# Optimization experiments

Hardware: AMD Instinct MI355X
Metric: run time of the kernel (lower is better)

Reference implementation:

```python
import jax, jax.numpy as jnp
import numpy as np

N_VOX = 200000
C_IN = 64
C_OUT = 128
GRID = (480, 360, 32)  # (D, H, W) cylindrical voxel grid
LRELU_SLOPE = 0.01
BN_EPS = 1e-5

OFFSETS_31 = [(dz, 0, dx) for dz in (-1, 0, 1) for dx in (-1, 0, 1)]  # kernel (3,1,3)
OFFSETS_13 = [(0, dy, dx) for dy in (-1, 0, 1) for dx in (-1, 0, 1)]  # kernel (1,3,3)


def _build_neighbors(coords, offsets, grid):
    """coords: [N,3] int. Returns [K,N] int32 neighbor indices, N = sentinel (inactive)."""
    D, H, W = grid
    n = coords.shape[0]
    lookup = np.full(D * H * W, -1, dtype=np.int64)
    lin = (coords[:, 0] * H + coords[:, 1]) * W + coords[:, 2]
    lookup[lin] = np.arange(n)
    nbrs = []
    for off in offsets:
        c = coords + np.asarray(off)
        valid = (c[:, 0] >= 0) & (c[:, 0] < D) & (c[:, 1] >= 0) & (c[:, 1] < H) & (c[:, 2] >= 0) & (c[:, 2] < W)
        l = np.clip((c[:, 0] * H + c[:, 1]) * W + c[:, 2], 0, D * H * W - 1)
        idx = np.where(valid, lookup[l], -1)
        nbrs.append(np.where(idx < 0, n, idx))
    return np.stack(nbrs).astype(np.int32)


def setup_inputs() -> dict:
    key = jax.random.key(0)
    ks = jax.random.split(key, 8)
    rng = np.random.default_rng(0)
    D, H, W = GRID
    lin = rng.choice(D * H * W, size=N_VOX, replace=False)
    coords = np.stack([lin // (H * W), (lin // W) % H, lin % W], axis=1)
    nbr31 = jnp.asarray(_build_neighbors(coords, OFFSETS_31, GRID))
    nbr13 = jnp.asarray(_build_neighbors(coords, OFFSETS_13, GRID))

    def kaiming(k, kk, cin, cout):
        return jax.random.normal(k, (kk, cin, cout), jnp.float32) * np.float32(1.0 / np.sqrt(kk * cin))

    return {
        "features": jax.random.normal(ks[0], (N_VOX, C_IN), jnp.float32),
        "nbr31": nbr31,
        "nbr13": nbr13,
        "W_conv1": kaiming(ks[1], 9, C_IN, C_OUT),
        "W_conv1_2": kaiming(ks[2], 9, C_OUT, C_OUT),
        "W_conv2": kaiming(ks[3], 9, C_IN, C_OUT),
        "W_conv3": kaiming(ks[4], 9, C_OUT, C_OUT),
        "g0": jnp.ones((C_OUT,), jnp.float32), "b0": jnp.zeros((C_OUT,), jnp.float32),
        "g0_2": jnp.ones((C_OUT,), jnp.float32), "b0_2": jnp.zeros((C_OUT,), jnp.float32),
        "g1": jnp.ones((C_OUT,), jnp.float32), "b1": jnp.zeros((C_OUT,), jnp.float32),
        "g2": jnp.ones((C_OUT,), jnp.float32), "b2": jnp.zeros((C_OUT,), jnp.float32),
    }


def _submconv(f, nbr, W):
    """Submanifold sparse conv: f [N,Cin], nbr [K,N] (N=sentinel), W [K,Cin,Cout]."""
    f_pad = jnp.concatenate([f, jnp.zeros((1, f.shape[1]), f.dtype)], axis=0)
    out = jnp.zeros((f.shape[0], W.shape[2]), f.dtype)
    for k in range(W.shape[0]):  # fixed K=9 kernel taps
        out = out + f_pad[nbr[k]] @ W[k]
    return out


def _lrelu(x):
    return jnp.where(x >= 0, x, LRELU_SLOPE * x)


def _bn(x, g, b):
    # BatchNorm1d, training mode: batch stats over active voxels (biased var)
    m = jnp.mean(x, axis=0)
    v = jnp.var(x, axis=0)
    return (x - m) * jax.lax.rsqrt(v + BN_EPS) * g + b


def reference(features, nbr31, nbr13, W_conv1, W_conv1_2, W_conv2, W_conv3,
              g0, b0, g0_2, b0_2, g1, b1, g2, b2):
    # shortcut branch: conv3x1 -> lrelu -> bn -> conv1x3 -> lrelu -> bn
    s = _submconv(features, nbr31, W_conv1)
    s = _bn(_lrelu(s), g0, b0)
    s = _submconv(s, nbr13, W_conv1_2)
    s = _bn(_lrelu(s), g0_2, b0_2)
    # main branch: conv1x3 -> lrelu -> bn -> conv3x1 -> lrelu -> bn
    r = _submconv(features, nbr13, W_conv2)
    r = _bn(_lrelu(r), g1, b1)
    r = _submconv(r, nbr31, W_conv3)
    r = _bn(_lrelu(r), g2, b2)
    return r + s
```

## Files before the change

kernel.cpp:

```cpp
#include <hip/hip_runtime.h>
#include <hip/hip_bf16.h>

typedef unsigned short u16;
typedef unsigned int u32;
typedef __attribute__((ext_vector_type(8))) short s16x8;
typedef __attribute__((ext_vector_type(4))) short s16x4;
typedef __attribute__((ext_vector_type(4))) float f32x4;

__device__ inline u16 f2bf(float x) {
    u32 u = __float_as_uint(x);
    u32 r = (u + 0x7fffu + ((u >> 16) & 1u)) >> 16;
    return (u16)r;
}
__device__ inline float bf2f(u16 u) {
    return __uint_as_float(((u32)u) << 16);
}

__global__ void k_feat2bf(const float* __restrict__ f, u16* __restrict__ o,
                          int total, int nvalid) {
    int i = (blockIdx.x * 256 + threadIdx.x) * 8;
    if (i >= total) return;
    s16x8 v;
#pragma unroll
    for (int j = 0; j < 8; ++j) {
        float x = (i + j < nvalid) ? f[i + j] : 0.f;
        v[j] = (short)f2bf(x);
    }
    *(s16x8*)(o + i) = v;
}

__global__ void k_swz(const float* __restrict__ W, u16* __restrict__ o, int cin) {
    int i = blockIdx.x * 256 + threadIdx.x;
    int total = 9 * cin * 128;
    if (i >= total) return;
    int j = i & 7;
    int l = (i >> 3) & 63;
    int fr = i >> 9;
    int ct = fr & 7;
    int rest = fr >> 3;
    int kcn = cin >> 5;
    int kc = rest % kcn;
    int t = rest / kcn;
    int kk = kc * 32 + (l >> 4) * 8 + j;
    int c = ct * 16 + (l & 15);
    o[i] = f2bf(W[(t * cin + kk) * 128 + c]);
}

template <int CIN>
__global__ __launch_bounds__(1024, 4) void k_conv(
    const u16* __restrict__ srcA, const u16* __restrict__ srcB,
    const int* __restrict__ nbrA, const int* __restrict__ nbrB,
    const u16* __restrict__ wA, const u16* __restrict__ wB,
    u16* __restrict__ zoutA, u16* __restrict__ zoutB,
    float* __restrict__ statsA, float* __restrict__ statsB,
    int N) {
    constexpr int KC = CIN / 32;
    constexpr int FR = 9 * KC * 2;
    __shared__ u16 wl[FR * 512];
    __shared__ float sstat[64];

    const int nvr = (N + 511) >> 9;
    const int npairs = 2 * nvr;
    const int i = blockIdx.x;
    const int c8 = i & 7;
    const int m = i >> 3;
    const int h = m & 3;
    const int q = m >> 2;
    const int p = 8 * q + c8;
    if (p >= npairs) return;
    const int vr = p % nvr;
    const int cz = p / nvr;
    const int half = h;

    const u16* __restrict__ src = cz ? srcB : srcA;
    const int* __restrict__ nbr = cz ? nbrB : nbrA;
    const u16* __restrict__ w = cz ? wB : wA;
    u16* __restrict__ zout = cz ? zoutB : zoutA;
    float* __restrict__ stats = cz ? statsB : statsA;

    const int tid = threadIdx.x;

    for (int ii = tid; ii < FR * 64; ii += 1024) {
        int pp = ii & 63;
        int f = ii >> 6;
        int ctp = f & 1;
        int tk = f >> 1;
        s16x8 v = *(const s16x8*)(w + ((size_t)(tk * 8 + half * 2 + ctp)) * 512 + pp * 8);
        *(s16x8*)&wl[(size_t)f * 512 + pp * 8] = v;
    }
    if (tid < 64) sstat[tid] = 0.f;
    __syncthreads();

    const int lane = tid & 63;
    const int wv = tid >> 6;
    const int base = vr * 512 + wv * 32;
    const int am = lane & 15;
    const int grp = lane >> 4;
    const int vi0 = base + am;
    const int vi1 = base + 16 + am;

    int r0[9], r1[9];
#pragma unroll
    for (int t = 0; t < 9; ++t) {
        r0[t] = (vi0 < N) ? nbr[t * N + vi0] : N;
        r1[t] = (vi1 < N) ? nbr[t * N + vi1] : N;
    }

    f32x4 acc0[2], acc1[2];
#pragma unroll
    for (int c = 0; c < 2; ++c) {
        acc0[c] = (f32x4){0.f, 0.f, 0.f, 0.f};
        acc1[c] = (f32x4){0.f, 0.f, 0.f, 0.f};
    }

#pragma unroll
    for (int t = 0; t < 9; ++t) {
        if (__any((r0[t] != N) || (r1[t] != N))) {
            const u16* sp0 = src + (size_t)r0[t] * CIN + grp * 8;
            const u16* sp1 = src + (size_t)r1[t] * CIN + grp * 8;
            s16x8 a0[KC], a1[KC];
#pragma unroll
            for (int kc = 0; kc < KC; ++kc) {
                a0[kc] = *(const s16x8*)(sp0 + kc * 32);
                a1[kc] = *(const s16x8*)(sp1 + kc * 32);
            }
            const u16* lb = wl + (size_t)t * (KC * 2) * 512 + lane * 8;
#pragma unroll
            for (int kc = 0; kc < KC; ++kc) {
#pragma unroll
                for (int c = 0; c < 2; ++c) {
                    s16x8 b = *(const s16x8*)(lb + (kc * 2 + c) * 512);
                    acc0[c] = __builtin_amdgcn_mfma_f32_16x16x32_bf16(a0[kc], b, acc0[c], 0, 0, 0);
                    acc1[c] = __builtin_amdgcn_mfma_f32_16x16x32_bf16(a1[kc], b, acc1[c], 0, 0, 0);
                }
            }
        }
    }

#pragma unroll
    for (int c = 0; c < 2; ++c) {
        float s = 0.f, qq = 0.f;
        const int col = half * 32 + c * 16 + am;
#pragma unroll
        for (int j = 0; j < 4; ++j) {
            {
                float x = acc0[c][j];
                float z = (x > 0.f) ? x : 0.01f * x;
                int row = base + grp * 4 + j;
                if (row < N) zout[(size_t)row * 128 + col] = f2bf(z);
                s += z;
                qq += z * z;
            }
            {
                float x = acc1[c][j];
                float z = (x > 0.f) ? x : 0.01f * x;
                int row = base + 16 + grp * 4 + j;
                if (row < N) zout[(size_t)row * 128 + col] = f2bf(z);
                s += z;
                qq += z * z;
            }
        }
        s += __shfl_xor(s, 16);
        qq += __shfl_xor(qq, 16);
        s += __shfl_xor(s, 32);
        qq += __shfl_xor(qq, 32);
        if (lane < 16) {
            atomicAdd(&sstat[c * 16 + am], s);
            atomicAdd(&sstat[32 + c * 16 + am], qq);
        }
    }
    __syncthreads();
    if (tid < 32) {
        int cg = half * 32 + tid;
        atomicAdd(stats + cg, sstat[tid]);
        atomicAdd(stats + 128 + cg, sstat[32 + tid]);
    }
}

__global__ void k_fin(const float* __restrict__ stats,
                      const float* __restrict__ g0, const float* __restrict__ b0,
                      const float* __restrict__ g1, const float* __restrict__ b1,
                      float* __restrict__ ss, int N) {
    int tid = threadIdx.x;
    int set = tid >> 7, c = tid & 127;
    const float* st = stats + set * 256;
    float invN = 1.f / (float)N;
    float m = st[c] * invN;
    float var = st[128 + c] * invN - m * m;
    const float* g = set ? g1 : g0;
    const float* b = set ? b1 : b0;
    float sc = g[c] * rsqrtf(var + 1e-5f);
    float sh = b[c] - m * sc;
    float* o = ss + set * 256;
    o[c] = sc;
    o[128 + c] = sh;
}

__global__ void k_aff(const u16* __restrict__ z, const float* __restrict__ ss,
                      u16* __restrict__ y, int N) {
    int v = blockIdx.x * 256 + threadIdx.x;
    int total = (N + 1) * 16;
    if (v >= total) return;
    int row = v >> 4;
    int cb = (v & 15) * 8;
    s16x8 o;
    if (row < N) {
        s16x8 zi = *(const s16x8*)(z + (size_t)row * 128 + cb);
#pragma unroll
        for (int j = 0; j < 8; ++j) {
            float x = bf2f((u16)zi[j]);
            float r = x * ss[cb + j] + ss[128 + cb + j];
            o[j] = (short)f2bf(r);
        }
    } else {
        o = (s16x8){0, 0, 0, 0, 0, 0, 0, 0};
    }
    *(s16x8*)(y + (size_t)row * 128 + cb) = o;
}

__global__ void k_final(const u16* __restrict__ z3, const u16* __restrict__ z4,
                        const float* __restrict__ ssA, const float* __restrict__ ssB,
                        float* __restrict__ out, int N) {
    int v = blockIdx.x * 256 + threadIdx.x;
    int total = N * 32;
    if (v >= total) return;
    int row = v >> 5;
    int cb = (v & 31) * 4;
    s16x4 a = *(const s16x4*)(z3 + (size_t)row * 128 + cb);
    s16x4 b = *(const s16x4*)(z4 + (size_t)row * 128 + cb);
    f32x4 o;
#pragma unroll
    for (int j = 0; j < 4; ++j) {
        int c = cb + j;
        o[j] = bf2f((u16)a[j]) * ssA[c] + ssA[128 + c] +
               bf2f((u16)b[j]) * ssB[c] + ssB[128 + c];
    }
    *(f32x4*)(out + (size_t)row * 128 + cb) = o;
}

extern "C" void kernel_launch(void* const* d_in, const int* in_sizes, int n_in,
                              void* d_out, int out_size, void* d_ws, size_t ws_size,
                              hipStream_t stream) {
    const float* feat = (const float*)d_in[0];
    const int* nbr31 = (const int*)d_in[1];
    const int* nbr13 = (const int*)d_in[2];
    const float* W1 = (const float*)d_in[3];
    const float* W12 = (const float*)d_in[4];
    const float* W2 = (const float*)d_in[5];
    const float* W3 = (const float*)d_in[6];
    const float* g0 = (const float*)d_in[7];
    const float* b0 = (const float*)d_in[8];
    const float* g02 = (const float*)d_in[9];
    const float* b02 = (const float*)d_in[10];
    const float* g1 = (const float*)d_in[11];
    const float* b1 = (const float*)d_in[12];
    const float* g2 = (const float*)d_in[13];
    const float* b2 = (const float*)d_in[14];
    float* out = (float*)d_out;
    const int N = in_sizes[0] / 64;

    char* p = (char*)d_ws;
    auto alloc = [&](size_t bytes) {
        char* r = p;
        p += (bytes + 255) & ~(size_t)255;
        return r;
    };
    float* stats = (float*)alloc(4 * 256 * sizeof(float));
    float* ss = (float*)alloc(4 * 256 * sizeof(float));
    u16* featbf = (u16*)alloc((size_t)(N + 1) * 64 * 2);
    u16* w1 = (u16*)alloc((size_t)9 * 64 * 128 * 2);
    u16* w2 = (u16*)alloc((size_t)9 * 64 * 128 * 2);
    u16* w12 = (u16*)alloc((size_t)9 * 128 * 128 * 2);
    u16* w3 = (u16*)alloc((size_t)9 * 128 * 128 * 2);
    u16* zA = (u16*)alloc((size_t)N * 128 * 2);
    u16* zB = (u16*)alloc((size_t)N * 128 * 2);
    u16* y1 = (u16*)alloc((size_t)(N + 1) * 128 * 2);
    u16* y2 = (u16*)alloc((size_t)(N + 1) * 128 * 2);

    hipMemsetAsync(stats, 0, 4 * 256 * sizeof(float), stream);

    int totF = (N + 1) * 64;
    k_feat2bf<<<(totF / 8 + 255) / 256, 256, 0, stream>>>(feat, featbf, totF, N * 64);
    k_swz<<<(9 * 64 * 128 + 255) / 256, 256, 0, stream>>>(W1, w1, 64);
    k_swz<<<(9 * 64 * 128 + 255) / 256, 256, 0, stream>>>(W2, w2, 64);
    k_swz<<<(9 * 128 * 128 + 255) / 256, 256, 0, stream>>>(W12, w12, 128);
    k_swz<<<(9 * 128 * 128 + 255) / 256, 256, 0, stream>>>(W3, w3, 128);

    int nvr = (N + 511) / 512;
    int npairs = 2 * nvr;
    int nblk = 8 * 4 * ((npairs + 7) / 8);

    k_conv<64><<<nblk, 1024, 0, stream>>>(
        featbf, featbf, nbr31, nbr13, w1, w2, zA, zB, stats + 0, stats + 256, N);
    k_fin<<<1, 256, 0, stream>>>(stats, g0, b0, g1, b1, ss, N);
    int ablk = ((N + 1) * 16 + 255) / 256;
    k_aff<<<ablk, 256, 0, stream>>>(zA, ss + 0, y1, N);
    k_aff<<<ablk, 256, 0, stream>>>(zB, ss + 256, y2, N);
    k_conv<128><<<nblk, 1024, 0, stream>>>(
        y1, y2, nbr13, nbr31, w12, w3, zA, zB, stats + 512, stats + 768, N);
    k_fin<<<1, 256, 0, stream>>>(stats + 512, g02, b02, g2, b2, ss + 512, N);
    k_final<<<(N * 32 + 255) / 256, 256, 0, stream>>>(zA, zB, ss + 512, ss + 768, out, N);
}
```

Before: 407.0 us.

## Drop LDS weight staging, use small 64-voxel blocks covering all output channels

Each conv block now handles 64 voxels across all 128 output channels: 8 waves split into 4 channel tiles times 2 voxel halves, on a 2D grid with one column per conv branch. Weights are read straight from global memory (through the cache) instead of being staged into LDS, and neighbor indices are loaded one tap ahead instead of all nine up front. The aim is to remove the per-block LDS weight copy and the 4x re-gather of source rows across channel-half blocks, and to lower register pressure so occupancy rises. The cost is more global and L2 traffic for weights, more blocks, and more global stat atomics.

```diff
diff --git a/kernel.cpp b/kernel.cpp
--- a/kernel.cpp
+++ b/kernel.cpp
@@ -47,7 +47,7 @@
 }
 
 template <int CIN>
-__global__ __launch_bounds__(1024, 4) void k_conv(
+__global__ __launch_bounds__(512, 7) void k_conv(
     const u16* __restrict__ srcA, const u16* __restrict__ srcB,
     const int* __restrict__ nbrA, const int* __restrict__ nbrB,
     const u16* __restrict__ wA, const u16* __restrict__ wB,
@@ -55,56 +55,29 @@
     float* __restrict__ statsA, float* __restrict__ statsB,
     int N) {
     constexpr int KC = CIN / 32;
-    constexpr int FR = 9 * KC * 2;
-    __shared__ u16 wl[FR * 512];
-    __shared__ float sstat[64];
-
-    const int nvr = (N + 511) >> 9;
-    const int npairs = 2 * nvr;
-    const int i = blockIdx.x;
-    const int c8 = i & 7;
-    const int m = i >> 3;
-    const int h = m & 3;
-    const int q = m >> 2;
-    const int p = 8 * q + c8;
-    if (p >= npairs) return;
-    const int vr = p % nvr;
-    const int cz = p / nvr;
-    const int half = h;
-
+    __shared__ float sstat[256];
+
+    const int tid = threadIdx.x;
+    const int cz = blockIdx.y;
     const u16* __restrict__ src = cz ? srcB : srcA;
     const int* __restrict__ nbr = cz ? nbrB : nbrA;
     const u16* __restrict__ w = cz ? wB : wA;
     u16* __restrict__ zout = cz ? zoutB : zoutA;
     float* __restrict__ stats = cz ? statsB : statsA;
 
-    const int tid = threadIdx.x;
-
-    for (int ii = tid; ii < FR * 64; ii += 1024) {
-        int pp = ii & 63;
-        int f = ii >> 6;
-        int ctp = f & 1;
-        int tk = f >> 1;
-        s16x8 v = *(const s16x8*)(w + ((size_t)(tk * 8 + half * 2 + ctp)) * 512 + pp * 8);
-        *(s16x8*)&wl[(size_t)f * 512 + pp * 8] = v;
-    }
-    if (tid < 64) sstat[tid] = 0.f;
+    if (tid < 256) sstat[tid] = 0.f;
     __syncthreads();
 
     const int lane = tid & 63;
     const int wv = tid >> 6;
-    const int base = vr * 512 + wv * 32;
+    const int ctile = wv & 3;
+    const int vhalf = wv >> 2;
+    const int base = blockIdx.x * 64 + vhalf * 32;
     const int am = lane & 15;
     const int grp = lane >> 4;
     const int vi0 = base + am;
     const int vi1 = base + 16 + am;
-
-    int r0[9], r1[9];
-#pragma unroll
-    for (int t = 0; t < 9; ++t) {
-        r0[t] = (vi0 < N) ? nbr[t * N + vi0] : N;
-        r1[t] = (vi1 < N) ? nbr[t * N + vi1] : N;
-    }
+    const bool v0 = vi0 < N, v1 = vi1 < N;
 
     f32x4 acc0[2], acc1[2];
 #pragma unroll
@@ -113,34 +86,44 @@
         acc1[c] = (f32x4){0.f, 0.f, 0.f, 0.f};
     }
 
+    int rc0 = v0 ? nbr[vi0] : N;
+    int rc1 = v1 ? nbr[vi1] : N;
+
 #pragma unroll
     for (int t = 0; t < 9; ++t) {
-        if (__any((r0[t] != N) || (r1[t] != N))) {
-            const u16* sp0 = src + (size_t)r0[t] * CIN + grp * 8;
-            const u16* sp1 = src + (size_t)r1[t] * CIN + grp * 8;
+        int rn0 = N, rn1 = N;
+        if (t < 8) {
+            if (v0) rn0 = nbr[(t + 1) * N + vi0];
+            if (v1) rn1 = nbr[(t + 1) * N + vi1];
+        }
+        if (__any((rc0 != N) || (rc1 != N))) {
+            const u16* sp0 = src + (size_t)rc0 * CIN + grp * 8;
+            const u16* sp1 = src + (size_t)rc1 * CIN + grp * 8;
             s16x8 a0[KC], a1[KC];
 #pragma unroll
             for (int kc = 0; kc < KC; ++kc) {
                 a0[kc] = *(const s16x8*)(sp0 + kc * 32);
                 a1[kc] = *(const s16x8*)(sp1 + kc * 32);
             }
-            const u16* lb = wl + (size_t)t * (KC * 2) * 512 + lane * 8;
+            const u16* wp = w + ((size_t)(t * KC) * 8 + ctile * 2) * 512 + lane * 8;
 #pragma unroll
             for (int kc = 0; kc < KC; ++kc) {
 #pragma unroll
                 for (int c = 0; c < 2; ++c) {
-                    s16x8 b = *(const s16x8*)(lb + (kc * 2 + c) * 512);
+                    s16x8 b = *(const s16x8*)(wp + (size_t)(kc * 8 + c) * 512);
                     acc0[c] = __builtin_amdgcn_mfma_f32_16x16x32_bf16(a0[kc], b, acc0[c], 0, 0, 0);
                     acc1[c] = __builtin_amdgcn_mfma_f32_16x16x32_bf16(a1[kc], b, acc1[c], 0, 0, 0);
                 }
             }
         }
+        rc0 = rn0;
+        rc1 = rn1;
     }
 
 #pragma unroll
     for (int c = 0; c < 2; ++c) {
         float s = 0.f, qq = 0.f;
-        const int col = half * 32 + c * 16 + am;
+        const int col = ctile * 32 + c * 16 + am;
 #pragma unroll
         for (int j = 0; j < 4; ++j) {
             {
@@ -165,15 +148,14 @@
         s += __shfl_xor(s, 32);
         qq += __shfl_xor(qq, 32);
         if (lane < 16) {
-            atomicAdd(&sstat[c * 16 + am], s);
-            atomicAdd(&sstat[32 + c * 16 + am], qq);
+            atomicAdd(&sstat[col], s);
+            atomicAdd(&sstat[128 + col], qq);
         }
     }
     __syncthreads();
-    if (tid < 32) {
-        int cg = half * 32 + tid;
-        atomicAdd(stats + cg, sstat[tid]);
-        atomicAdd(stats + 128 + cg, sstat[32 + tid]);
+    if (tid < 128) {
+        atomicAdd(stats + tid, sstat[tid]);
+        atomicAdd(stats + 128 + tid, sstat[128 + tid]);
     }
 }
 
@@ -286,17 +268,14 @@
     k_swz<<<(9 * 128 * 128 + 255) / 256, 256, 0, stream>>>(W12, w12, 128);
     k_swz<<<(9 * 128 * 128 + 255) / 256, 256, 0, stream>>>(W3, w3, 128);
 
-    int nvr = (N + 511) / 512;
-    int npairs = 2 * nvr;
-    int nblk = 8 * 4 * ((npairs + 7) / 8);
-
-    k_conv<64><<<nblk, 1024, 0, stream>>>(
+    dim3 cgrid((N + 63) / 64, 2);
+    k_conv<64><<<cgrid, 512, 0, stream>>>(
         featbf, featbf, nbr31, nbr13, w1, w2, zA, zB, stats + 0, stats + 256, N);
     k_fin<<<1, 256, 0, stream>>>(stats, g0, b0, g1, b1, ss, N);
     int ablk = ((N + 1) * 16 + 255) / 256;
     k_aff<<<ablk, 256, 0, stream>>>(zA, ss + 0, y1, N);
     k_aff<<<ablk, 256, 0, stream>>>(zB, ss + 256, y2, N);
-    k_conv<128><<<nblk, 1024, 0, stream>>>(
+    k_conv<128><<<cgrid, 512, 0, stream>>>(
         y1, y2, nbr13, nbr31, w12, w3, zA, zB, stats + 512, stats + 768, N);
     k_fin<<<1, 256, 0, stream>>>(stats + 512, g02, b02, g2, b2, ss + 512, N);
     k_final<<<(N * 32 + 255) / 256, 256, 0, stream>>>(zA, zB, ss + 512, ss + 768, out, N);
```

Result: slower. 500.1 us (+22.9%).

## Software-pipeline neighbor gathers across taps and halve conv block size

Applied to the files above, without the earlier changes.

The conv kernel now double-buffers the A-operand gathers, loading the next tap's neighbor features (and the neighbor index two taps ahead) while the MFMAs for the current tap run. Before, all nine taps' indices were loaded up front and each tap's gather stalled before its MFMAs. Blocks shrink from 1024 to 512 threads, covering 256 voxels each, so each block stages the same weight slice for half as many voxels. The gathers are now unconditional, so all-empty taps still issue loads, and the doubled A buffers raise register pressure.

```diff
diff --git a/kernel.cpp b/kernel.cpp
--- a/kernel.cpp
+++ b/kernel.cpp
@@ -47,7 +47,7 @@
 }
 
 template <int CIN>
-__global__ __launch_bounds__(1024, 4) void k_conv(
+__global__ __launch_bounds__(512, 4) void k_conv(
     const u16* __restrict__ srcA, const u16* __restrict__ srcB,
     const int* __restrict__ nbrA, const int* __restrict__ nbrB,
     const u16* __restrict__ wA, const u16* __restrict__ wB,
@@ -59,7 +59,7 @@
     __shared__ u16 wl[FR * 512];
     __shared__ float sstat[64];
 
-    const int nvr = (N + 511) >> 9;
+    const int nvr = (N + 255) >> 8;
     const int npairs = 2 * nvr;
     const int i = blockIdx.x;
     const int c8 = i & 7;
@@ -80,7 +80,7 @@
 
     const int tid = threadIdx.x;
 
-    for (int ii = tid; ii < FR * 64; ii += 1024) {
+    for (int ii = tid; ii < FR * 64; ii += 512) {
         int pp = ii & 63;
         int f = ii >> 6;
         int ctp = f & 1;
@@ -93,17 +93,27 @@
 
     const int lane = tid & 63;
     const int wv = tid >> 6;
-    const int base = vr * 512 + wv * 32;
+    const int base = vr * 256 + wv * 32;
     const int am = lane & 15;
     const int grp = lane >> 4;
     const int vi0 = base + am;
     const int vi1 = base + 16 + am;
-
-    int r0[9], r1[9];
-#pragma unroll
-    for (int t = 0; t < 9; ++t) {
-        r0[t] = (vi0 < N) ? nbr[t * N + vi0] : N;
-        r1[t] = (vi1 < N) ? nbr[t * N + vi1] : N;
+    const bool v0 = vi0 < N, v1 = vi1 < N;
+
+    int rc0 = v0 ? nbr[vi0] : N;
+    int rc1 = v1 ? nbr[vi1] : N;
+    int rn0 = v0 ? nbr[N + vi0] : N;
+    int rn1 = v1 ? nbr[N + vi1] : N;
+
+    s16x8 a0[2][KC], a1[2][KC];
+    {
+        const u16* sp0 = src + (size_t)rc0 * CIN + grp * 8;
+        const u16* sp1 = src + (size_t)rc1 * CIN + grp * 8;
+#pragma unroll
+        for (int kc = 0; kc < KC; ++kc) {
+            a0[0][kc] = *(const s16x8*)(sp0 + kc * 32);
+            a1[0][kc] = *(const s16x8*)(sp1 + kc * 32);
+        }
     }
 
     f32x4 acc0[2], acc1[2];
@@ -115,26 +125,35 @@
 
 #pragma unroll
     for (int t = 0; t < 9; ++t) {
-        if (__any((r0[t] != N) || (r1[t] != N))) {
-            const u16* sp0 = src + (size_t)r0[t] * CIN + grp * 8;
-            const u16* sp1 = src + (size_t)r1[t] * CIN + grp * 8;
-            s16x8 a0[KC], a1[KC];
+        const int cur = t & 1, nxt = cur ^ 1;
+        if (t < 8) {
+            const u16* sp0 = src + (size_t)rn0 * CIN + grp * 8;
+            const u16* sp1 = src + (size_t)rn1 * CIN + grp * 8;
 #pragma unroll
             for (int kc = 0; kc < KC; ++kc) {
-                a0[kc] = *(const s16x8*)(sp0 + kc * 32);
-                a1[kc] = *(const s16x8*)(sp1 + kc * 32);
+                a0[nxt][kc] = *(const s16x8*)(sp0 + kc * 32);
+                a1[nxt][kc] = *(const s16x8*)(sp1 + kc * 32);
             }
+        }
+        int rf0 = N, rf1 = N;
+        if (t < 7) {
+            if (v0) rf0 = nbr[(t + 2) * N + vi0];
+            if (v1) rf1 = nbr[(t + 2) * N + vi1];
+        }
+        if (__any((rc0 != N) || (rc1 != N))) {
             const u16* lb = wl + (size_t)t * (KC * 2) * 512 + lane * 8;
 #pragma unroll
             for (int kc = 0; kc < KC; ++kc) {
 #pragma unroll
                 for (int c = 0; c < 2; ++c) {
                     s16x8 b = *(const s16x8*)(lb + (kc * 2 + c) * 512);
-                    acc0[c] = __builtin_amdgcn_mfma_f32_16x16x32_bf16(a0[kc], b, acc0[c], 0, 0, 0);
-                    acc1[c] = __builtin_amdgcn_mfma_f32_16x16x32_bf16(a1[kc], b, acc1[c], 0, 0, 0);
+                    acc0[c] = __builtin_amdgcn_mfma_f32_16x16x32_bf16(a0[cur][kc], b, acc0[c], 0, 0, 0);
+                    acc1[c] = __builtin_amdgcn_mfma_f32_16x16x32_bf16(a1[cur][kc], b, acc1[c], 0, 0, 0);
                 }
             }
         }
+        rc0 = rn0; rc1 = rn1;
+        rn0 = rf0; rn1 = rf1;
     }
 
 #pragma unroll
@@ -286,17 +305,17 @@
     k_swz<<<(9 * 128 * 128 + 255) / 256, 256, 0, stream>>>(W12, w12, 128);
     k_swz<<<(9 * 128 * 128 + 255) / 256, 256, 0, stream>>>(W3, w3, 128);
 
-    int nvr = (N + 511) / 512;
+    int nvr = (N + 255) / 256;
     int npairs = 2 * nvr;
     int nblk = 8 * 4 * ((npairs + 7) / 8);
 
-    k_conv<64><<<nblk, 1024, 0, stream>>>(
+    k_conv<64><<<nblk, 512, 0, stream>>>(
         featbf, featbf, nbr31, nbr13, w1, w2, zA, zB, stats + 0, stats + 256, N);
     k_fin<<<1, 256, 0, stream>>>(stats, g0, b0, g1, b1, ss, N);
     int ablk = ((N + 1) * 16 + 255) / 256;
     k_aff<<<ablk, 256, 0, stream>>>(zA, ss + 0, y1, N);
     k_aff<<<ablk, 256, 0, stream>>>(zB, ss + 256, y2, N);
-    k_conv<128><<<nblk, 1024, 0, stream>>>(
+    k_conv<128><<<nblk, 512, 0, stream>>>(
         y1, y2, nbr13, nbr31, w12, w3, zA, zB, stats + 512, stats + 768, N);
     k_fin<<<1, 256, 0, stream>>>(stats + 512, g02, b02, g2, b2, ss + 512, N);
     k_final<<<(N * 32 + 255) / 256, 256, 0, stream>>>(zA, zB, ss + 512, ss + 768, out, N);
```

After: 424.1 us. 1.04x slower.

## Give each wave 64 voxels with per-16-row tap skipping and prefetched neighbor indices

Applied to the files above, without the earlier changes.

The conv kernel now runs 512-thread blocks in which each wave covers 64 voxels as four 16-row MFMA groups instead of 32. Each weight fragment read from LDS therefore feeds four row groups rather than two. Neighbor indices are loaded one per lane and prefetched a tap ahead, then broadcast with shuffles, replacing the 18 index registers per lane. Empty taps are now skipped per 16-row group via a ballot mask rather than per wave. The trade-off is more accumulator and A-operand registers per lane, which could lower occupancy, plus extra shuffle and branch overhead.

```diff
diff --git a/kernel.cpp b/kernel.cpp
--- a/kernel.cpp
+++ b/kernel.cpp
@@ -3,6 +3,7 @@
 
 typedef unsigned short u16;
 typedef unsigned int u32;
+typedef unsigned long long u64;
 typedef __attribute__((ext_vector_type(8))) short s16x8;
 typedef __attribute__((ext_vector_type(4))) short s16x4;
 typedef __attribute__((ext_vector_type(4))) float f32x4;
@@ -47,7 +48,7 @@
 }
 
 template <int CIN>
-__global__ __launch_bounds__(1024, 4) void k_conv(
+__global__ __launch_bounds__(512, 4) void k_conv(
     const u16* __restrict__ srcA, const u16* __restrict__ srcB,
     const int* __restrict__ nbrA, const int* __restrict__ nbrB,
     const u16* __restrict__ wA, const u16* __restrict__ wB,
@@ -70,7 +71,7 @@
     if (p >= npairs) return;
     const int vr = p % nvr;
     const int cz = p / nvr;
-    const int half = h;
+    const int quarter = h;
 
     const u16* __restrict__ src = cz ? srcB : srcA;
     const int* __restrict__ nbr = cz ? nbrB : nbrA;
@@ -80,12 +81,12 @@
 
     const int tid = threadIdx.x;
 
-    for (int ii = tid; ii < FR * 64; ii += 1024) {
+    for (int ii = tid; ii < FR * 64; ii += 512) {
         int pp = ii & 63;
         int f = ii >> 6;
         int ctp = f & 1;
         int tk = f >> 1;
-        s16x8 v = *(const s16x8*)(w + ((size_t)(tk * 8 + half * 2 + ctp)) * 512 + pp * 8);
+        s16x8 v = *(const s16x8*)(w + ((size_t)(tk * 8 + quarter * 2 + ctp)) * 512 + pp * 8);
         *(s16x8*)&wl[(size_t)f * 512 + pp * 8] = v;
     }
     if (tid < 64) sstat[tid] = 0.f;
@@ -93,85 +94,110 @@
 
     const int lane = tid & 63;
     const int wv = tid >> 6;
-    const int base = vr * 512 + wv * 32;
+    const int base = vr * 512 + wv * 64;
     const int am = lane & 15;
     const int grp = lane >> 4;
-    const int vi0 = base + am;
-    const int vi1 = base + 16 + am;
-
-    int r0[9], r1[9];
+    const int vi = base + lane;
+    const bool vok = vi < N;
+
+    int rc = vok ? nbr[vi] : N;
+
+    f32x4 acc[4][2];
+#pragma unroll
+    for (int g = 0; g < 4; ++g)
+#pragma unroll
+        for (int c = 0; c < 2; ++c) acc[g][c] = (f32x4){0.f, 0.f, 0.f, 0.f};
+
 #pragma unroll
     for (int t = 0; t < 9; ++t) {
-        r0[t] = (vi0 < N) ? nbr[t * N + vi0] : N;
-        r1[t] = (vi1 < N) ? nbr[t * N + vi1] : N;
-    }
-
-    f32x4 acc0[2], acc1[2];
-#pragma unroll
-    for (int c = 0; c < 2; ++c) {
-        acc0[c] = (f32x4){0.f, 0.f, 0.f, 0.f};
-        acc1[c] = (f32x4){0.f, 0.f, 0.f, 0.f};
-    }
-
-#pragma unroll
-    for (int t = 0; t < 9; ++t) {
-        if (__any((r0[t] != N) || (r1[t] != N))) {
-            const u16* sp0 = src + (size_t)r0[t] * CIN + grp * 8;
-            const u16* sp1 = src + (size_t)r1[t] * CIN + grp * 8;
-            s16x8 a0[KC], a1[KC];
-#pragma unroll
-            for (int kc = 0; kc < KC; ++kc) {
-                a0[kc] = *(const s16x8*)(sp0 + kc * 32);
-                a1[kc] = *(const s16x8*)(sp1 + kc * 32);
-            }
-            const u16* lb = wl + (size_t)t * (KC * 2) * 512 + lane * 8;
-#pragma unroll
-            for (int kc = 0; kc < KC; ++kc) {
-#pragma unroll
-                for (int c = 0; c < 2; ++c) {
-                    s16x8 b = *(const s16x8*)(lb + (kc * 2 + c) * 512);
-                    acc0[c] = __builtin_amdgcn_mfma_f32_16x16x32_bf16(a0[kc], b, acc0[c], 0, 0, 0);
-                    acc1[c] = __builtin_amdgcn_mfma_f32_16x16x32_bf16(a1[kc], b, acc1[c], 0, 0, 0);
-                }
-            }
-        }
-    }
-
-#pragma unroll
-    for (int c = 0; c < 2; ++c) {
-        float s = 0.f, qq = 0.f;
-        const int col = half * 32 + c * 16 + am;
-#pragma unroll
-        for (int j = 0; j < 4; ++j) {
-            {
-                float x = acc0[c][j];
+        int rn = N;
+        if (t < 8 && vok) rn = nbr[(t + 1) * N + vi];
+
+        u64 mask = __ballot(rc != N);
+        const bool e0 = (mask & 0xFFFFull) != 0;
+        const bool e1 = (mask & 0xFFFF0000ull) != 0;
+        const bool e2 = (mask & 0xFFFF00000000ull) != 0;
+        const bool e3 = (mask & 0xFFFF000000000000ull) != 0;
+
+        s16x8 a[4][KC];
+        if (e0) {
+            int rg = __shfl(rc, am);
+            const u16* sp = src + (size_t)rg * CIN + grp * 8;
+#pragma unroll
+            for (int kc = 0; kc < KC; ++kc) a[0][kc] = *(const s16x8*)(sp + kc * 32);
+        }
+        if (e1) {
+            int rg = __shfl(rc, 16 + am);
+            const u16* sp = src + (size_t)rg * CIN + grp * 8;
+#pragma unroll
+            for (int kc = 0; kc < KC; ++kc) a[1][kc] = *(const s16x8*)(sp + kc * 32);
+        }
+        if (e2) {
+            int rg = __shfl(rc, 32 + am);
+            const u16* sp = src + (size_t)rg * CIN + grp * 8;
+#pragma unroll
+            for (int kc = 0; kc < KC; ++kc) a[2][kc] = *(const s16x8*)(sp + kc * 32);
+        }
+        if (e3) {
+            int rg = __shfl(rc, 48 + am);
+            const u16* sp = src + (size_t)rg * CIN + grp * 8;
+#pragma unroll
+            for (int kc = 0; kc < KC; ++kc) a[3][kc] = *(const s16x8*)(sp + kc * 32);
+        }
+
+        const u16* lb = wl + (size_t)t * (KC * 2) * 512 + lane * 8;
+#pragma unroll
+        for (int kc = 0; kc < KC; ++kc) {
+            s16x8 b0 = *(const s16x8*)(lb + (size_t)(kc * 2 + 0) * 512);
+            s16x8 b1 = *(const s16x8*)(lb + (size_t)(kc * 2 + 1) * 512);
+            if (e0) {
+                acc[0][0] = __builtin_amdgcn_mfma_f32_16x16x32_bf16(a[0][kc], b0, acc[0][0], 0, 0, 0);
+                acc[0][1] = __builtin_amdgcn_mfma_f32_16x16x32_bf16(a[0][kc], b1, acc[0][1], 0, 0, 0);
+            }
+            if (e1) {
+                acc[1][0] = __builtin_amdgcn_mfma_f32_16x16x32_bf16(a[1][kc], b0, acc[1][0], 0, 0, 0);
+                acc[1][1] = __builtin_amdgcn_mfma_f32_16x16x32_bf16(a[1][kc], b1, acc[1][1], 0, 0, 0);
+            }
+            if (e2) {
+                acc[2][0] = __builtin_amdgcn_mfma_f32_16x16x32_bf16(a[2][kc], b0, acc[2][0], 0, 0, 0);
+                acc[2][1] = __builtin_amdgcn_mfma_f32_16x16x32_bf16(a[2][kc], b1, acc[2][1], 0, 0, 0);
+            }
+            if (e3) {
+                acc[3][0] = __builtin_amdgcn_mfma_f32_16x16x32_bf16(a[3][kc], b0, acc[3][0], 0, 0, 0);
+                acc[3][1] = __builtin_amdgcn_mfma_f32_16x16x32_bf16(a[3][kc], b1, acc[3][1], 0, 0, 0);
+            }
+        }
+        rc = rn;
+    }
+
+#pragma unroll
+    for (int g = 0; g < 4; ++g) {
+#pragma unroll
+        for (int c = 0; c < 2; ++c) {
+            float s = 0.f, qq = 0.f;
+            const int col = quarter * 32 + c * 16 + am;
+#pragma unroll
+            for (int j = 0; j < 4; ++j) {
+                float x = acc[g][c][j];
                 float z = (x > 0.f) ? x : 0.01f * x;
-                int row = base + grp * 4 + j;
+                int row = base + g * 16 + grp * 4 + j;
                 if (row < N) zout[(size_t)row * 128 + col] = f2bf(z);
                 s += z;
                 qq += z * z;
             }
-            {
-                float x = acc1[c][j];
-                float z = (x > 0.f) ? x : 0.01f * x;
-                int row = base + 16 + grp * 4 + j;
-                if (row < N) zout[(size_t)row * 128 + col] = f2bf(z);
-                s += z;
-                qq += z * z;
-            }
-        }
-        s += __shfl_xor(s, 16);
-        qq += __shfl_xor(qq, 16);
-        s += __shfl_xor(s, 32);
-        qq += __shfl_xor(qq, 32);
-        if (lane < 16) {
-            atomicAdd(&sstat[c * 16 + am], s);
-            atomicAdd(&sstat[32 + c * 16 + am], qq);
+            s += __shfl_xor(s, 16);
+            qq += __shfl_xor(qq, 16);
+            s += __shfl_xor(s, 32);
+            qq += __shfl_xor(qq, 32);
+            if (lane < 16) {
+                atomicAdd(&sstat[c * 16 + am], s);
+                atomicAdd(&sstat[32 + c * 16 + am], qq);
+            }
         }
     }
     __syncthreads();
     if (tid < 32) {
-        int cg = half * 32 + tid;
+        int cg = quarter * 32 + tid;
         atomicAdd(stats + cg, sstat[tid]);
         atomicAdd(stats + 128 + cg, sstat[32 + tid]);
     }
@@ -290,13 +316,13 @@
     int npairs = 2 * nvr;
     int nblk = 8 * 4 * ((npairs + 7) / 8);
 
-    k_conv<64><<<nblk, 1024, 0, stream>>>(
+    k_conv<64><<<nblk, 512, 0, stream>>>(
         featbf, featbf, nbr31, nbr13, w1, w2, zA, zB, stats + 0, stats + 256, N);
     k_fin<<<1, 256, 0, stream>>>(stats, g0, b0, g1, b1, ss, N);
     int ablk = ((N + 1) * 16 + 255) / 256;
     k_aff<<<ablk, 256, 0, stream>>>(zA, ss + 0, y1, N);
     k_aff<<<ablk, 256, 0, stream>>>(zB, ss + 256, y2, N);
-    k_conv<128><<<nblk, 1024, 0, stream>>>(
+    k_conv<128><<<nblk, 512, 0, stream>>>(
         y1, y2, nbr13, nbr31, w12, w3, zA, zB, stats + 512, stats + 768, N);
     k_fin<<<1, 256, 0, stream>>>(stats + 512, g02, b02, g2, b2, ss + 512, N);
     k_final<<<(N * 32 + 255) / 256, 256, 0, stream>>>(zA, zB, ss + 512, ss + 768, out, N);
```

Result: no change. 401.3 us (-1.4%).
